# Kernel tuning notes

Measured on AMD Instinct MI355X. Metric: run time of the kernel, lower is better.

Reference implementation:

```python
import jax, jax.numpy as jnp
import numpy as np

B, F_DENSE, F_SPARSE, E, V = 16384, 13, 26, 16, 100000
HID = [512, 256]
BN_EPS = 1e-5


def setup_inputs() -> dict:
    key = jax.random.key(0)
    ks = jax.random.split(key, 20)
    d_in = (F_DENSE + F_SPARSE) * E  # 624
    inp = {
        "Xi": jax.random.randint(ks[0], (B, F_DENSE + F_SPARSE, 1), 0, V, dtype=jnp.int64 if jax.config.read("jax_enable_x64") else jnp.int32).astype(jnp.int32),
        "Xv": jax.random.uniform(ks[1], (B, F_DENSE + F_SPARSE), dtype=jnp.float32),
        # first-order grouped conv (per dense field: weight (E,), bias (E,))
        "W1": jax.random.normal(ks[2], (F_DENSE, E), jnp.float32) * 0.05,
        "b1": jax.random.normal(ks[3], (F_DENSE, E), jnp.float32) * 0.05,
        # first-order embedding tables (26, V, E)
        "emb1": jax.random.normal(ks[4], (F_SPARSE, V, E), jnp.float32) * 0.01,
        # second-order grouped conv + tables
        "W2": jax.random.normal(ks[5], (F_DENSE, E), jnp.float32) * 0.05,
        "b2": jax.random.normal(ks[6], (F_DENSE, E), jnp.float32) * 0.05,
        "emb2": jax.random.normal(ks[7], (F_SPARSE, V, E), jnp.float32) * 0.01,
        # deep MLP (eval-mode BN: running_mean=0, running_var=1)
        "Lw1": jax.random.normal(ks[8], (d_in, HID[0]), jnp.float32) * (1.0 / np.sqrt(d_in)),
        "Lb1": jnp.zeros((HID[0],), jnp.float32),
        "g1": jnp.ones((HID[0],), jnp.float32),
        "be1": jnp.zeros((HID[0],), jnp.float32),
        "Lw2": jax.random.normal(ks[9], (HID[0], HID[1]), jnp.float32) * (1.0 / np.sqrt(HID[0])),
        "Lb2": jnp.zeros((HID[1],), jnp.float32),
        "g2": jnp.ones((HID[1],), jnp.float32),
        "be2": jnp.zeros((HID[1],), jnp.float32),
        # the per-sample random bias created inside the torch forward, fixed here
        "bias": jax.random.normal(ks[10], (B,), jnp.float32),
    }
    return inp


def reference(Xi, Xv, W1, b1, emb1, W2, b2, emb2,
              Lw1, Lb1, g1, be1, Lw2, Lb2, g2, be2, bias):
    xi_dense = Xi[:, :F_DENSE, 0].astype(jnp.float32)      # (B,13)
    idx = Xi[:, F_DENSE:, 0]                               # (B,26) int
    xv_d = Xv[:, :F_DENSE]                                 # (B,13)
    xv_s = Xv[:, F_DENSE:]                                 # (B,26)

    tbl = jnp.arange(F_SPARSE)[None, :]                    # (1,26)

    # ---- FM first order ----
    # grouped 1x1 conv == per-field affine of the dense scalar, then scale by Xv
    first_lin = (xi_dense[:, :, None] * W1 + b1) * xv_d[:, :, None]   # (B,13,E)
    first_emb = emb1[tbl, idx] * xv_s[:, :, None]                     # (B,26,E) gather
    fm_first = jnp.concatenate([first_lin.reshape(B, -1),
                                first_emb.reshape(B, -1)], axis=1)    # (B,39E)

    # ---- FM second order ----
    sec_lin = xi_dense[:, :, None] * W2 + b2                          # (B,13,E) (no Xv scale, as in source)
    sec_emb = emb2[tbl, idx] * xv_s[:, :, None]                       # (B,26,E)

    sum_emb = sec_lin.sum(axis=1) + sec_emb.sum(axis=1)               # (B,E)
    sumsq = (sec_lin * sec_lin).sum(axis=1) + (sec_emb * sec_emb).sum(axis=1)
    fm_second = (sum_emb * sum_emb - sumsq) * 0.5                     # (B,E)

    # ---- deep part (eval-mode BN, dropout off) ----
    h = jnp.concatenate([sec_lin.reshape(B, -1), sec_emb.reshape(B, -1)], axis=1)  # (B,39E)
    inv = jnp.float32(1.0 / np.sqrt(1.0 + BN_EPS))
    h = (h @ Lw1 + Lb1) * inv * g1 + be1
    h = (h @ Lw2 + Lb2) * inv * g2 + be2

    total = fm_first.sum(axis=1) + fm_second.sum(axis=1) + h.sum(axis=1) + bias
    return total
```

## Files before the change

### kernel.cpp

```cpp
#include <hip/hip_runtime.h>
#include <hip/hip_bf16.h>


#define B_     16384
#define FD_    13
#define FS_    26
#define F_     39
#define E_     16
#define V_     100000
#define H1_    512
#define H2_    256
#define DIN_   624
#define INV_   0.9999950000374998f


__global__ void k_v2(const float* __restrict__ Lw2, const float* __restrict__ g2,
                     float* __restrict__ v2) {
    int i = blockIdx.x;
    int l = threadIdx.x;
    float acc = 0.f;
#pragma unroll
    for (int t = 0; t < 4; ++t) {
        int j = t * 64 + l;
        acc += Lw2[i * H2_ + j] * g2[j];
    }
#pragma unroll
    for (int off = 32; off >= 1; off >>= 1)
        acc += __shfl_xor(acc, off, 64);
    if (l == 0) v2[i] = acc * INV_;
}

__global__ void k_weff(const float* __restrict__ Lw1, const float* __restrict__ g1,
                       const float* __restrict__ v2, float* __restrict__ w_eff) {
    __shared__ float red[4];
    int k = blockIdx.x;
    int t = threadIdx.x;
    float acc = Lw1[k * H1_ + t]       * g1[t]       * v2[t]
              + Lw1[k * H1_ + t + 256] * g1[t + 256] * v2[t + 256];
#pragma unroll
    for (int off = 32; off >= 1; off >>= 1)
        acc += __shfl_xor(acc, off, 64);
    if ((t & 63) == 0) red[t >> 6] = acc;
    __syncthreads();
    if (t == 0)
        w_eff[k] = (red[0] + red[1] + red[2] + red[3]) * INV_;
}

__global__ void k_scalar(const float* __restrict__ Lb1, const float* __restrict__ g1,
                         const float* __restrict__ be1, const float* __restrict__ v2,
                         const float* __restrict__ Lb2, const float* __restrict__ g2,
                         const float* __restrict__ be2, float* __restrict__ scalarC) {
    __shared__ float red[8];
    int t = threadIdx.x;
    float val = (Lb1[t] * INV_ * g1[t] + be1[t]) * v2[t];
    if (t < H2_)
        val += Lb2[t] * INV_ * g2[t] + be2[t];
#pragma unroll
    for (int off = 32; off >= 1; off >>= 1)
        val += __shfl_xor(val, off, 64);
    if ((t & 63) == 0) red[t >> 6] = val;
    __syncthreads();
    if (t == 0) {
        float s = 0.f;
#pragma unroll
        for (int w = 0; w < 8; ++w) s += red[w];
        scalarC[0] = s;
    }
}

__global__ void k_main(const int*   __restrict__ Xi,
                       const float* __restrict__ Xv,
                       const float* __restrict__ W1,  const float* __restrict__ b1,
                       const float* __restrict__ emb1,
                       const float* __restrict__ W2,  const float* __restrict__ b2,
                       const float* __restrict__ emb2,
                       const float* __restrict__ bias,
                       const float* __restrict__ w_eff,
                       const float* __restrict__ scalarC,
                       float* __restrict__ out) {
    int t = blockIdx.x * 256 + threadIdx.x;
    int b = t >> 4;
    int e = t & 15;

    const int*   xi_row = Xi + b * F_;
    const float* xv_row = Xv + b * F_;

    float accF = 0.f;
    float s1   = 0.f;
    float s2   = 0.f;
    float accH = 0.f;

#pragma unroll
    for (int f = 0; f < FD_; ++f) {
        float xi  = (float)xi_row[f];
        float xv  = xv_row[f];
        float w1v = W1[f * E_ + e];
        float b1v = b1[f * E_ + e];
        float w2v = W2[f * E_ + e];
        float b2v = b2[f * E_ + e];
        float fl  = (xi * w1v + b1v) * xv;
        float sec = xi * w2v + b2v;
        accF += fl;
        s1   += sec;
        s2   += sec * sec;
        accH += sec * w_eff[f * E_ + e];
    }

#pragma unroll
    for (int f = 0; f < FS_; ++f) {
        int   id = xi_row[FD_ + f];
        float xv = xv_row[FD_ + f];
        float e1 = emb1[(f * V_ + id) * E_ + e];
        float e2 = emb2[(f * V_ + id) * E_ + e];
        float sec = e2 * xv;
        accF += e1 * xv;
        s1   += sec;
        s2   += sec * sec;
        accH += sec * w_eff[(FD_ + f) * E_ + e];
    }

    float part = accF + accH + 0.5f * (s1 * s1 - s2);
    part += __shfl_xor(part, 8, 16);
    part += __shfl_xor(part, 4, 16);
    part += __shfl_xor(part, 2, 16);
    part += __shfl_xor(part, 1, 16);

    if (e == 0)
        out[b] = part + bias[b] + scalarC[0];
}

extern "C" void kernel_launch(void* const* d_in, const int* in_sizes, int n_in,
                              void* d_out, int out_size, void* d_ws, size_t ws_size,
                              hipStream_t stream) {
    const int*   Xi   = (const int*)  d_in[0];
    const float* Xv   = (const float*)d_in[1];
    const float* W1   = (const float*)d_in[2];
    const float* b1   = (const float*)d_in[3];
    const float* emb1 = (const float*)d_in[4];
    const float* W2   = (const float*)d_in[5];
    const float* b2   = (const float*)d_in[6];
    const float* emb2 = (const float*)d_in[7];
    const float* Lw1  = (const float*)d_in[8];
    const float* Lb1  = (const float*)d_in[9];
    const float* g1   = (const float*)d_in[10];
    const float* be1  = (const float*)d_in[11];
    const float* Lw2  = (const float*)d_in[12];
    const float* Lb2  = (const float*)d_in[13];
    const float* g2   = (const float*)d_in[14];
    const float* be2  = (const float*)d_in[15];
    const float* bias = (const float*)d_in[16];
    float* out = (float*)d_out;

    float* ws      = (float*)d_ws;
    float* v2      = ws;
    float* w_eff   = ws + 512;
    float* scalarC = ws + 512 + 624;

    k_v2    <<<H1_,  64, 0, stream>>>(Lw2, g2, v2);
    k_weff  <<<DIN_, 256, 0, stream>>>(Lw1, g1, v2, w_eff);
    k_scalar<<<1,    512, 0, stream>>>(Lb1, g1, be1, v2, Lb2, g2, be2, scalarC);
    k_main  <<<(B_ * E_) / 256, 256, 0, stream>>>(
        Xi, Xv, W1, b1, emb1, W2, b2, emb2, bias, w_eff, scalarC, out);
}
```

Before: 320.6 us.

## Vectorize embedding gathers with float4 and stage row inputs in LDS

Each sample row is now handled by 4 threads, each loading float4 slices of the embedding rows, in place of 16 threads each loading one scalar. The small weight tables, w_eff and the block's Xi/Xv rows are staged in shared memory first. This is meant to cut the number of gather instructions and the redundant per-thread index loads. The grid changes to 512 blocks of 128 threads, which gives fewer threads in flight to hide the random-gather latency.

```diff
diff --git a/kernel.cpp b/kernel.cpp
--- a/kernel.cpp
+++ b/kernel.cpp
@@ -12,6 +12,9 @@
 #define H2_    256
 #define DIN_   624
 #define INV_   0.9999950000374998f
+
+#define ROWS_PB 32
+#define TPB     128
 
 
 __global__ void k_v2(const float* __restrict__ Lw2, const float* __restrict__ g2,
@@ -68,65 +71,95 @@
     }
 }
 
-__global__ void k_main(const int*   __restrict__ Xi,
-                       const float* __restrict__ Xv,
-                       const float* __restrict__ W1,  const float* __restrict__ b1,
-                       const float* __restrict__ emb1,
-                       const float* __restrict__ W2,  const float* __restrict__ b2,
-                       const float* __restrict__ emb2,
-                       const float* __restrict__ bias,
-                       const float* __restrict__ w_eff,
-                       const float* __restrict__ scalarC,
-                       float* __restrict__ out) {
-    int t = blockIdx.x * 256 + threadIdx.x;
-    int b = t >> 4;
-    int e = t & 15;
+__global__ __launch_bounds__(TPB) void k_main(
+        const int*   __restrict__ Xi,
+        const float* __restrict__ Xv,
+        const float* __restrict__ W1,  const float* __restrict__ b1,
+        const float* __restrict__ emb1,
+        const float* __restrict__ W2,  const float* __restrict__ b2,
+        const float* __restrict__ emb2,
+        const float* __restrict__ bias,
+        const float* __restrict__ w_eff,
+        const float* __restrict__ scalarC,
+        float* __restrict__ out) {
+    __shared__ __align__(16) float sTab[832 + DIN_];
+    __shared__ int   sXi[ROWS_PB * F_];
+    __shared__ float sXv[ROWS_PB * F_];
 
-    const int*   xi_row = Xi + b * F_;
-    const float* xv_row = Xv + b * F_;
+    const int tid = threadIdx.x;
+    const int r   = tid & 3;
+    const int rl  = tid >> 2;
+    const int row = blockIdx.x * ROWS_PB + rl;
 
-    float accF = 0.f;
-    float s1   = 0.f;
-    float s2   = 0.f;
-    float accH = 0.f;
+    for (int i = tid; i < 208; i += TPB) {
+        sTab[i]       = W1[i];
+        sTab[208 + i] = b1[i];
+        sTab[416 + i] = W2[i];
+        sTab[624 + i] = b2[i];
+    }
+    for (int i = tid; i < DIN_; i += TPB)
+        sTab[832 + i] = w_eff[i];
+    {
+        const int base = blockIdx.x * ROWS_PB * F_;
+        for (int i = tid; i < ROWS_PB * F_; i += TPB) {
+            sXi[i] = Xi[base + i];
+            sXv[i] = Xv[base + i];
+        }
+    }
+    __syncthreads();
+
+    const float4* tab4   = (const float4*)sTab;
+    const float4* emb1_4 = (const float4*)emb1;
+    const float4* emb2_4 = (const float4*)emb2;
+
+    float aFx = 0.f, aFy = 0.f, aFz = 0.f, aFw = 0.f;
+    float s1x = 0.f, s1y = 0.f, s1z = 0.f, s1w = 0.f;
+    float s2x = 0.f, s2y = 0.f, s2z = 0.f, s2w = 0.f;
+    float aHx = 0.f, aHy = 0.f, aHz = 0.f, aHw = 0.f;
 
 #pragma unroll
     for (int f = 0; f < FD_; ++f) {
-        float xi  = (float)xi_row[f];
-        float xv  = xv_row[f];
-        float w1v = W1[f * E_ + e];
-        float b1v = b1[f * E_ + e];
-        float w2v = W2[f * E_ + e];
-        float b2v = b2[f * E_ + e];
-        float fl  = (xi * w1v + b1v) * xv;
-        float sec = xi * w2v + b2v;
-        accF += fl;
-        s1   += sec;
-        s2   += sec * sec;
-        accH += sec * w_eff[f * E_ + e];
+        float  xi = (float)sXi[rl * F_ + f];
+        float  xv = sXv[rl * F_ + f];
+        float4 w1 = tab4[f * 4 + r];
+        float4 bb1 = tab4[52 + f * 4 + r];
+        float4 w2 = tab4[104 + f * 4 + r];
+        float4 bb2 = tab4[156 + f * 4 + r];
+        float4 we = tab4[208 + f * 4 + r];
+        float secx = xi * w2.x + bb2.x, secy = xi * w2.y + bb2.y;
+        float secz = xi * w2.z + bb2.z, secw = xi * w2.w + bb2.w;
+        aFx += (xi * w1.x + bb1.x) * xv;  aFy += (xi * w1.y + bb1.y) * xv;
+        aFz += (xi * w1.z + bb1.z) * xv;  aFw += (xi * w1.w + bb1.w) * xv;
+        s1x += secx; s1y += secy; s1z += secz; s1w += secw;
+        s2x += secx * secx; s2y += secy * secy; s2z += secz * secz; s2w += secw * secw;
+        aHx += secx * we.x; aHy += secy * we.y; aHz += secz * we.z; aHw += secw * we.w;
     }
 
 #pragma unroll
     for (int f = 0; f < FS_; ++f) {
-        int   id = xi_row[FD_ + f];
-        float xv = xv_row[FD_ + f];
-        float e1 = emb1[(f * V_ + id) * E_ + e];
-        float e2 = emb2[(f * V_ + id) * E_ + e];
-        float sec = e2 * xv;
-        accF += e1 * xv;
-        s1   += sec;
-        s2   += sec * sec;
-        accH += sec * w_eff[(FD_ + f) * E_ + e];
+        int    id = sXi[rl * F_ + FD_ + f];
+        float  xv = sXv[rl * F_ + FD_ + f];
+        size_t o  = (size_t)(f * V_ + id) * 4 + r;
+        float4 e1 = emb1_4[o];
+        float4 e2 = emb2_4[o];
+        float4 we = tab4[208 + (FD_ + f) * 4 + r];
+        float secx = e2.x * xv, secy = e2.y * xv, secz = e2.z * xv, secw = e2.w * xv;
+        aFx += e1.x * xv; aFy += e1.y * xv; aFz += e1.z * xv; aFw += e1.w * xv;
+        s1x += secx; s1y += secy; s1z += secz; s1w += secw;
+        s2x += secx * secx; s2y += secy * secy; s2z += secz * secz; s2w += secw * secw;
+        aHx += secx * we.x; aHy += secy * we.y; aHz += secz * we.z; aHw += secw * we.w;
     }
 
-    float part = accF + accH + 0.5f * (s1 * s1 - s2);
-    part += __shfl_xor(part, 8, 16);
-    part += __shfl_xor(part, 4, 16);
-    part += __shfl_xor(part, 2, 16);
-    part += __shfl_xor(part, 1, 16);
+    float part = (aFx + aHx + 0.5f * (s1x * s1x - s2x))
+               + (aFy + aHy + 0.5f * (s1y * s1y - s2y))
+               + (aFz + aHz + 0.5f * (s1z * s1z - s2z))
+               + (aFw + aHw + 0.5f * (s1w * s1w - s2w));
 
-    if (e == 0)
-        out[b] = part + bias[b] + scalarC[0];
+    part += __shfl_xor(part, 1, 4);
+    part += __shfl_xor(part, 2, 4);
+
+    if (r == 0)
+        out[row] = part + bias[row] + scalarC[0];
 }
 
 extern "C" void kernel_launch(void* const* d_in, const int* in_sizes, int n_in,
@@ -159,6 +192,6 @@
     k_v2    <<<H1_,  64, 0, stream>>>(Lw2, g2, v2);
     k_weff  <<<DIN_, 256, 0, stream>>>(Lw1, g1, v2, w_eff);
     k_scalar<<<1,    512, 0, stream>>>(Lb1, g1, be1, v2, Lb2, g2, be2, scalarC);
-    k_main  <<<(B_ * E_) / 256, 256, 0, stream>>>(
+    k_main  <<<B_ / ROWS_PB, TPB, 0, stream>>>(
         Xi, Xv, W1, b1, emb1, W2, b2, emb2, bias, w_eff, scalarC, out);
 }
```

Result: no change. 326.6 us (+1.9%).

## Bucket-sort sparse indices per field to localize embedding gathers

Applied to the files above, without the earlier changes.

Replaces the single gather kernel with three stages. A per-field bucket sort of indices groups rows by table region. A gather kernel then walks the sorted order, loads float4 embedding rows and accumulates per-row partials with atomics into a scratch buffer. A final kernel combines the dense fields, the scratch vectors and the FM square term per row. The aim is better cache and DRAM locality on random embedding lookups, at the cost of extra kernel launches, a 26-block sort with low parallelism, scratch writes and reads, and atomics.

```diff
diff --git a/kernel.cpp b/kernel.cpp
--- a/kernel.cpp
+++ b/kernel.cpp
@@ -11,7 +11,10 @@
 #define H1_    512
 #define H2_    256
 #define DIN_   624
+#define NBKT   64
 #define INV_   0.9999950000374998f
+
+typedef unsigned int uint_t;
 
 
 __global__ void k_v2(const float* __restrict__ Lw2, const float* __restrict__ g2,
@@ -68,65 +71,147 @@
     }
 }
 
-__global__ void k_main(const int*   __restrict__ Xi,
-                       const float* __restrict__ Xv,
-                       const float* __restrict__ W1,  const float* __restrict__ b1,
-                       const float* __restrict__ emb1,
-                       const float* __restrict__ W2,  const float* __restrict__ b2,
-                       const float* __restrict__ emb2,
-                       const float* __restrict__ bias,
-                       const float* __restrict__ w_eff,
-                       const float* __restrict__ scalarC,
-                       float* __restrict__ out) {
-    int t = blockIdx.x * 256 + threadIdx.x;
-    int b = t >> 4;
-    int e = t & 15;
-
-    const int*   xi_row = Xi + b * F_;
-    const float* xv_row = Xv + b * F_;
-
-    float accF = 0.f;
-    float s1   = 0.f;
-    float s2   = 0.f;
-    float accH = 0.f;
+__global__ __launch_bounds__(256) void k_sort(const int* __restrict__ Xi,
+                                              uint_t* __restrict__ sorted,
+                                              uint_t* __restrict__ bstart,
+                                              float*  __restrict__ lin) {
+    __shared__ uint_t cnt[NBKT];
+    __shared__ uint_t off[NBKT + 1];
+    __shared__ uint_t cur[NBKT];
+    const int f   = blockIdx.x;
+    const int tid = threadIdx.x;
+
+    for (int i = blockIdx.x * 256 + tid; i < B_; i += 26 * 256)
+        lin[i] = 0.f;
+
+    if (tid < NBKT) cnt[tid] = 0;
+    __syncthreads();
+    for (int row = tid; row < B_; row += 256) {
+        uint_t id = (uint_t)Xi[row * F_ + FD_ + f];
+        atomicAdd(&cnt[(id * (uint_t)NBKT) / (uint_t)V_], 1u);
+    }
+    __syncthreads();
+    if (tid == 0) {
+        uint_t a = 0;
+        for (int b = 0; b < NBKT; ++b) { off[b] = a; a += cnt[b]; }
+        off[NBKT] = a;
+    }
+    __syncthreads();
+    if (tid < NBKT) cur[tid] = off[tid];
+    if (tid < NBKT + 1) bstart[f * (NBKT + 1) + tid] = off[tid];
+    __syncthreads();
+    for (int row = tid; row < B_; row += 256) {
+        uint_t id = (uint_t)Xi[row * F_ + FD_ + f];
+        uint_t b  = (id * (uint_t)NBKT) / (uint_t)V_;
+        uint_t pos = atomicAdd(&cur[b], 1u);
+        sorted[f * B_ + pos] = ((uint_t)row << 17) | id;
+    }
+}
+
+__global__ __launch_bounds__(256) void k_gather(
+        const float* __restrict__ Xv,
+        const float* __restrict__ emb1, const float* __restrict__ emb2,
+        const float* __restrict__ w_eff,
+        const uint_t* __restrict__ sorted, const uint_t* __restrict__ bstart,
+        float* __restrict__ lin, float* __restrict__ scratch) {
+    const int f = blockIdx.x >> 6;
+    const int b = blockIdx.x & (NBKT - 1);
+    const uint_t start = bstart[f * (NBKT + 1) + b];
+    const uint_t end   = bstart[f * (NBKT + 1) + b + 1];
+    const int r    = threadIdx.x & 3;
+    const int slot = threadIdx.x >> 2;
+
+    const float4* e1t = (const float4*)emb1;
+    const float4* e2t = (const float4*)emb2;
+    const float4  wq  = ((const float4*)w_eff)[(FD_ + f) * 4 + r];
+    float4* scr4 = (float4*)scratch;
+
+    for (uint_t i = start + slot; i < end; i += 64) {
+        uint_t packed = sorted[f * B_ + i];
+        int row = (int)(packed >> 17);
+        int id  = (int)(packed & 0x1FFFFu);
+        float xv = Xv[row * F_ + FD_ + f];
+        size_t o = (size_t)(f * V_ + id) * 4 + r;
+        float4 e1 = e1t[o];
+        float4 e2 = e2t[o];
+        float4 sec;
+        sec.x = e2.x * xv; sec.y = e2.y * xv; sec.z = e2.z * xv; sec.w = e2.w * xv;
+        float p = e1.x * xv + sec.x * wq.x - 0.5f * sec.x * sec.x
+                + e1.y * xv + sec.y * wq.y - 0.5f * sec.y * sec.y
+                + e1.z * xv + sec.z * wq.z - 0.5f * sec.z * sec.z
+                + e1.w * xv + sec.w * wq.w - 0.5f * sec.w * sec.w;
+        p += __shfl_xor(p, 1, 4);
+        p += __shfl_xor(p, 2, 4);
+        if (r == 0) atomicAdd(&lin[row], p);
+        scr4[(size_t)(f * B_ + row) * 4 + r] = sec;
+    }
+}
+
+__global__ __launch_bounds__(256) void k_final(
+        const int* __restrict__ Xi, const float* __restrict__ Xv,
+        const float* __restrict__ W1, const float* __restrict__ b1,
+        const float* __restrict__ W2, const float* __restrict__ b2,
+        const float* __restrict__ w_eff, const float* __restrict__ scalarC,
+        const float* __restrict__ lin, const float* __restrict__ scratch,
+        const float* __restrict__ bias, float* __restrict__ out) {
+    __shared__ __align__(16) float sTab[832 + 208];
+    const int tid = threadIdx.x;
+    for (int i = tid; i < 208; i += 256) {
+        sTab[i]       = W1[i];
+        sTab[208 + i] = b1[i];
+        sTab[416 + i] = W2[i];
+        sTab[624 + i] = b2[i];
+        sTab[832 + i] = w_eff[i];
+    }
+    __syncthreads();
+
+    const int row = blockIdx.x * 256 + tid;
+    const float4* st4  = (const float4*)sTab;
+    const float4* scr4 = (const float4*)scratch;
+
+    float4 s1q[4];
+#pragma unroll
+    for (int q = 0; q < 4; ++q) { s1q[q].x = 0.f; s1q[q].y = 0.f; s1q[q].z = 0.f; s1q[q].w = 0.f; }
+    float acc = lin[row];
 
 #pragma unroll
     for (int f = 0; f < FD_; ++f) {
-        float xi  = (float)xi_row[f];
-        float xv  = xv_row[f];
-        float w1v = W1[f * E_ + e];
-        float b1v = b1[f * E_ + e];
-        float w2v = W2[f * E_ + e];
-        float b2v = b2[f * E_ + e];
-        float fl  = (xi * w1v + b1v) * xv;
-        float sec = xi * w2v + b2v;
-        accF += fl;
-        s1   += sec;
-        s2   += sec * sec;
-        accH += sec * w_eff[f * E_ + e];
+        float xi = (float)Xi[row * F_ + f];
+        float xv = Xv[row * F_ + f];
+#pragma unroll
+        for (int q = 0; q < 4; ++q) {
+            float4 w1  = st4[f * 4 + q];
+            float4 bb1 = st4[52 + f * 4 + q];
+            float4 w2  = st4[104 + f * 4 + q];
+            float4 bb2 = st4[156 + f * 4 + q];
+            float4 wq  = st4[208 + f * 4 + q];
+            float4 sec;
+            sec.x = xi * w2.x + bb2.x; sec.y = xi * w2.y + bb2.y;
+            sec.z = xi * w2.z + bb2.z; sec.w = xi * w2.w + bb2.w;
+            acc += (xi * w1.x + bb1.x) * xv + (xi * w1.y + bb1.y) * xv
+                 + (xi * w1.z + bb1.z) * xv + (xi * w1.w + bb1.w) * xv;
+            acc += sec.x * wq.x + sec.y * wq.y + sec.z * wq.z + sec.w * wq.w;
+            acc -= 0.5f * (sec.x * sec.x + sec.y * sec.y + sec.z * sec.z + sec.w * sec.w);
+            s1q[q].x += sec.x; s1q[q].y += sec.y; s1q[q].z += sec.z; s1q[q].w += sec.w;
+        }
     }
 
 #pragma unroll
     for (int f = 0; f < FS_; ++f) {
-        int   id = xi_row[FD_ + f];
-        float xv = xv_row[FD_ + f];
-        float e1 = emb1[(f * V_ + id) * E_ + e];
-        float e2 = emb2[(f * V_ + id) * E_ + e];
-        float sec = e2 * xv;
-        accF += e1 * xv;
-        s1   += sec;
-        s2   += sec * sec;
-        accH += sec * w_eff[(FD_ + f) * E_ + e];
-    }
-
-    float part = accF + accH + 0.5f * (s1 * s1 - s2);
-    part += __shfl_xor(part, 8, 16);
-    part += __shfl_xor(part, 4, 16);
-    part += __shfl_xor(part, 2, 16);
-    part += __shfl_xor(part, 1, 16);
-
-    if (e == 0)
-        out[b] = part + bias[b] + scalarC[0];
+#pragma unroll
+        for (int q = 0; q < 4; ++q) {
+            float4 s = scr4[(size_t)(f * B_ + row) * 4 + q];
+            s1q[q].x += s.x; s1q[q].y += s.y; s1q[q].z += s.z; s1q[q].w += s.w;
+        }
+    }
+
+    float s1sq = 0.f;
+#pragma unroll
+    for (int q = 0; q < 4; ++q)
+        s1sq += s1q[q].x * s1q[q].x + s1q[q].y * s1q[q].y
+              + s1q[q].z * s1q[q].z + s1q[q].w * s1q[q].w;
+
+    out[row] = acc + 0.5f * s1sq + bias[row] + scalarC[0];
 }
 
 extern "C" void kernel_launch(void* const* d_in, const int* in_sizes, int n_in,
@@ -151,14 +236,21 @@
     const float* bias = (const float*)d_in[16];
     float* out = (float*)d_out;
 
-    float* ws      = (float*)d_ws;
-    float* v2      = ws;
-    float* w_eff   = ws + 512;
-    float* scalarC = ws + 512 + 624;
+    float*  ws      = (float*)d_ws;
+    float*  v2      = ws;
+    float*  w_eff   = ws + 512;
+    float*  scalarC = ws + 1136;
+    float*  lin     = ws + 1152;
+    uint_t* bstart  = (uint_t*)(ws + 17536);
+    uint_t* sorted  = (uint_t*)(ws + 19232);
+    float*  scratch = ws + 19232 + 425984;
 
     k_v2    <<<H1_,  64, 0, stream>>>(Lw2, g2, v2);
     k_weff  <<<DIN_, 256, 0, stream>>>(Lw1, g1, v2, w_eff);
     k_scalar<<<1,    512, 0, stream>>>(Lb1, g1, be1, v2, Lb2, g2, be2, scalarC);
-    k_main  <<<(B_ * E_) / 256, 256, 0, stream>>>(
-        Xi, Xv, W1, b1, emb1, W2, b2, emb2, bias, w_eff, scalarC, out);
-}
+    k_sort  <<<FS_,  256, 0, stream>>>(Xi, sorted, bstart, lin);
+    k_gather<<<FS_ * NBKT, 256, 0, stream>>>(Xv, emb1, emb2, w_eff, sorted,
+                                             bstart, lin, scratch);
+    k_final <<<B_ / 256, 256, 0, stream>>>(Xi, Xv, W1, b1, W2, b2, w_eff,
+                                           scalarC, lin, scratch, bias, out);
+}
```

Measured after the change: 405.6 us. 1.27x slower.
